# Optimization experiments

Hardware: AMD Instinct MI355X
Metric: run time of the kernel (lower is better)

The kernel has to match this reference:

```python
import jax, jax.numpy as jnp
import numpy as np

N_QUBITS = 10
DIM = 2 ** N_QUBITS          # quantum state dimension
N_LAYERS = 8                 # QAOA circuit depth
B, D_IN, D_HID = 8192, 1024, 2048


def _build_hamiltonians(key):
    """Faithful to _create_cost_hamiltonian / _create_mixer_hamiltonian."""
    k1, k2 = jax.random.split(key)
    # cost: random diagonal * 0.1 plus 100 nearest-neighbour real couplings * 0.05
    diag = (jax.random.normal(k1, (DIM,)) * 0.1).astype(jnp.complex64)
    Hc = jnp.zeros((DIM, DIM), jnp.complex64).at[jnp.arange(DIM), jnp.arange(DIM)].set(diag)
    i = jnp.arange(100)
    j = (i + 1) % DIM
    c = (jax.random.normal(k2, (100,)) * 0.05).astype(jnp.complex64)
    Hc = Hc.at[i, j].set(c).at[j, i].set(jnp.conj(c))
    # mixer: sum of Pauli-X on every qubit -> H[i, i^(1<<q)] += 1
    idx = jnp.arange(DIM)
    Hm = jnp.zeros((DIM, DIM), jnp.complex64)
    for q in range(N_QUBITS):
        Hm = Hm.at[idx, idx ^ (1 << q)].add(1.0)
    return Hc, Hm


def setup_inputs() -> dict:
    key = jax.random.key(0)
    ks = jax.random.split(key, 8)
    Hc, Hm = _build_hamiltonians(ks[0])
    s = lambda k, *sh: jax.random.normal(k, sh, jnp.float32)
    return {
        "x": s(ks[1], B, D_IN),
        "W1": s(ks[2], D_IN, D_HID) * 0.02, "b1": jnp.zeros((D_HID,), jnp.float32),
        "W2": s(ks[3], D_HID, D_HID // 2) * 0.02, "b2": jnp.zeros((D_HID // 2,), jnp.float32),
        "Wq": s(ks[4], N_QUBITS, D_HID // 2) * 0.02, "bq": jnp.zeros((D_HID // 2,), jnp.float32),
        "Wo": s(ks[5], D_HID // 2, D_IN) * 0.02, "bo": jnp.zeros((D_IN,), jnp.float32),
        "circuit_params": s(ks[6], 2 * N_LAYERS),
        "Hc": Hc, "Hm": Hm,
    }


def _qaoa_params(circuit_params, Hc, Hm):
    """QuantumApproximateOptimizer.optimize_parameters: layered unitary evolution
    then a projective measurement mapped to +/-1 parameters."""
    state = jnp.full((DIM,), 1.0 / np.sqrt(DIM), jnp.complex64)
    for l in range(N_LAYERS):  # small fixed layer count -> Python loop OK
        gamma = circuit_params[2 * l].astype(jnp.complex64)
        beta = circuit_params[2 * l + 1].astype(jnp.complex64)
        state = jax.scipy.linalg.expm(-1j * gamma * Hc) @ state
        state = jax.scipy.linalg.expm(-1j * beta * Hm) @ state
    probs = jnp.abs(state) ** 2
    m = jax.random.categorical(jax.random.key(42), jnp.log(probs + 1e-30))
    # format(m, '0{n}b') is MSB-first
    bits = (m >> jnp.arange(N_QUBITS - 1, -1, -1)) & 1
    return bits.astype(jnp.float32) * 2.0 - 1.0  # +/-1 per qubit


def reference(x, W1, b1, W2, b2, Wq, bq, Wo, bo, circuit_params, Hc, Hm):
    # classical encoder: Linear -> ReLU -> Linear
    feat = jax.nn.relu(x @ W1 + b1) @ W2 + b2          # [B, D_HID//2]
    # quantum branch (batch independent)
    qp = _qaoa_params(circuit_params, Hc, Hm)          # [N_QUBITS]
    # surface-code error correction: correction_lookup only maps syndromes
    # '0000'/'1111' to qubit indices 23/24, which fail the `qubit_idx < param_dim`
    # guard for param_dim = N_QUBITS -> provably a no-op; qp unchanged.
    qf = qp @ Wq + bq                                  # [D_HID//2]
    return (feat + qf) @ Wo + bo                       # [B, D_IN]
```

## Files before the change

kernel.cpp:

```cpp
#include <hip/hip_runtime.h>
#include <hip/hip_bf16.h>
#include <stdint.h>

#define DIM 1024
#define NQ 10
#define NLAYERS 8
#define KTAYLOR 16
#define B_ROWS 8192
#define D_IN 1024
#define D_HID 2048
#define D_HALF 1024

typedef __bf16 bf16x8 __attribute__((ext_vector_type(8)));
typedef float f32x4 __attribute__((ext_vector_type(4)));

__device__ __forceinline__ float ldany(const void* p, size_t i, bool f32) {
  if (f32) return ((const float*)p)[i];
  return (float)((const __bf16*)p)[i];
}

__device__ __forceinline__ uint16_t f2bf_bits(float f) {
  __bf16 v = (__bf16)f;
  return *(uint16_t*)&v;
}

__device__ __forceinline__ uint32_t rotl32(uint32_t v, int d) {
  return (v << d) | (v >> (32 - d));
}

__device__ inline void threefry2x32(uint32_t k0, uint32_t k1, uint32_t& x0, uint32_t& x1) {
  uint32_t ks2 = k0 ^ k1 ^ 0x1BD11BDAu;
  x0 += k0; x1 += k1;
#define RND(r) { x0 += x1; x1 = rotl32(x1, r); x1 ^= x0; }
  RND(13) RND(15) RND(26) RND(6)
  x0 += k1; x1 += ks2 + 1u;
  RND(17) RND(29) RND(16) RND(24)
  x0 += ks2; x1 += k0 + 2u;
  RND(13) RND(15) RND(26) RND(6)
  x0 += k0; x1 += k1 + 3u;
  RND(17) RND(29) RND(16) RND(24)
  x0 += k1; x1 += ks2 + 4u;
  RND(13) RND(15) RND(26) RND(6)
  x0 += ks2; x1 += k0 + 5u;
#undef RND
}

__device__ __forceinline__ float gumbel_from_bits(uint32_t b) {
  float f = __uint_as_float((b >> 9) | 0x3f800000u) - 1.0f;
  float u = fmaxf(f, 1.17549435e-38f);
  return -__logf(-__logf(u));
}

struct cplx { double r, i; };
__device__ __forceinline__ cplx load_hc(const void* H, int code, size_t idx) {
  switch (code) {
    case 2: return {(double)((const float*)H)[idx], 0.0};
    case 3: {
      const uint16_t* h = (const uint16_t*)H;
      return {(double)__uint_as_float((uint32_t)h[2 * idx] << 16),
              (double)__uint_as_float((uint32_t)h[2 * idx + 1] << 16)};
    }
    case 4: {
      const double* d = (const double*)H;
      return {d[2 * idx], d[2 * idx + 1]};
    }
    default: {
      float2 v = ((const float2*)H)[idx];
      return {(double)v.x, (double)v.y};
    }
  }
}

__global__ __launch_bounds__(1024) void detect_prep(
    const uint32_t* __restrict__ w1raw, const uint32_t* __restrict__ hc,
    int hcb, const void* __restrict__ b1, const void* __restrict__ bo,
    int* __restrict__ flags, float* __restrict__ b1f,
    float* __restrict__ bias0, float* __restrict__ bias2W) {
  __shared__ int cnt_sh;
  __shared__ int f0_sh;
  const int t = threadIdx.x;
  if (t == 0) cnt_sh = 0;
  __syncthreads();
  if (t < 256) {
    uint16_t h = (uint16_t)(w1raw[t] & 0xFFFFu);
    if (((h >> 7) & 0xFF) >= 0x80) atomicAdd(&cnt_sh, 1);
  }
  __syncthreads();
  if (t == 0) {
    f0_sh = (cnt_sh > 32) ? 1 : 0;
    flags[0] = f0_sh;
    uint32_t w1 = hc[1] & 0x7FFFFFFFu;
    uint32_t w2 = hc[2] & 0x7FFFFFFFu;
    uint32_t w1025 = hc[1025] & 0x7FFFFFFFu;
    int code;
    if (w2 != 0u) code = 1;
    else if (w1 != 0u && (w1 >> 16) == 0u) code = 3;
    else if (w1025 != 0u) code = 2;
    else if (w1 != 0u) code = 4;
    else code = 0;
    flags[1] = code;
  }
  {
    size_t d = (size_t)t * 1025;
    uint32_t a = 0;
    if (8 * d + 4 <= (size_t)hcb) a += hc[2 * d];
    if (4 * d + 4 <= (size_t)hcb) a += hc[d];
    if (16 * d + 4 <= (size_t)hcb) a += hc[4 * d];
    asm volatile("" :: "v"(a));
  }
  __syncthreads();
  const bool f32 = (f0_sh != 0);
  b1f[t] = ldany(b1, t, f32);
  b1f[t + 1024] = ldany(b1, t + 1024, f32);
  bias0[t] = 0.f;
  if (t < 1024) bias0[t + 1024] = 0.f;
  if (t < 1024) bias2W[t] = ldany(bo, t, f32);
}

__global__ void sentinel_kernel(const int* __restrict__ flags,
                                const int* __restrict__ diag,
                                float* __restrict__ out) {
  if (threadIdx.x == 0 && (diag[0] || flags[1] == 0)) {
    out[0] = 1048576.0f + 4194304.0f * (float)diag[0]
           + 65536.0f * (float)flags[1] + 16.0f * (float)diag[1];
  }
}

__device__ void qaoa_body(char* smem,
    const void* __restrict__ Hc_raw, const void* __restrict__ cp,
    const void* __restrict__ b2, const void* __restrict__ bq,
    const void* __restrict__ Wq, const int* __restrict__ flags,
    float* __restrict__ bias2, int* __restrict__ diag) {
  double2* X   = (double2*)smem;
  double* gtab = (double*)(smem + 16384);
  double* cbt  = gtab + 8;
  double* sbt  = cbt + 8;
  float* redv  = (float*)(sbt + 8);
  float* redp  = redv + 4;
  int*   redi  = (int*)(redp + 4);
  int*   bmsh  = redi + 4;

  const int t = threadIdx.x;
  const int lane = t & 63, w = t >> 6;
  const bool f32 = (flags[0] != 0);
  const int code = flags[1];

  double dgr[4], dgi[4];
#pragma unroll
  for (int j = 0; j < 4; ++j) {
    size_t e = (size_t)(w * 256 + j * 64 + lane);
    cplx d = load_hc(Hc_raw, code, e * DIM + e);
    dgr[j] = d.r; dgi[j] = d.i;
  }
  double u0r = 0, u0i = 0, c0r = 0, c0i = 0;
  double u1r = 0, u1i = 0, c1r = 0, c1i = 0;
  if (w == 0) {
    const int e0 = lane, e1 = 64 + lane;
    { cplx u = load_hc(Hc_raw, code, (size_t)e0 * DIM + e0 + 1); u0r = u.r; u0i = u.i; }
    if (e0 >= 1)  { cplx c = load_hc(Hc_raw, code, (size_t)e0 * DIM + e0 - 1); c0r = c.r; c0i = c.i; }
    if (e1 <= 100){ cplx u = load_hc(Hc_raw, code, (size_t)e1 * DIM + e1 + 1); u1r = u.r; u1i = u.i; }
    if (e1 <= 101){ cplx c = load_hc(Hc_raw, code, (size_t)e1 * DIM + e1 - 1); c1r = c.r; c1i = c.i; }
  }
  if (t < NLAYERS) {
    gtab[t] = (double)ldany(cp, 2 * t, f32);
    double b = (double)ldany(cp, 2 * t + 1, f32), s, c;
    sincos(b, &s, &c);
    cbt[t] = c; sbt[t] = s;
  }
  double ar[4], ai[4];
#pragma unroll
  for (int j = 0; j < 4; ++j) { ar[j] = 0.03125; ai[j] = 0.0; }
  __syncthreads();

  for (int l = 0; l < NLAYERS; ++l) {
    const double gamma = gtab[l];
    const double cb = cbt[l], sb = sbt[l];
    const double cb2 = cb * cb, cbsb = cb * sb, sb2 = sb * sb;

    if (w == 0) {
      double p0r = ar[0], p0i = ai[0], p1r = ar[1], p1i = ai[1];
      double y0r = p0r, y0i = p0i, y1r = p1r, y1i = p1i;
#pragma unroll
      for (int k = 1; k <= KTAYLOR; ++k) {
        double a0r = __shfl_down(p0r, 1), a0i = __shfl_down(p0i, 1);
        double a1r = __shfl_down(p1r, 1), a1i = __shfl_down(p1i, 1);
        double m0r = __shfl_up(p0r, 1),   m0i = __shfl_up(p0i, 1);
        double m1r = __shfl_up(p1r, 1),   m1i = __shfl_up(p1i, 1);
        double b0r = __shfl(p1r, 0),  b0i = __shfl(p1i, 0);
        double b1r = __shfl(p0r, 63), b1i = __shfl(p0i, 63);
        if (lane == 63) { a0r = b0r; a0i = b0i; }
        if (lane == 0)  { m1r = b1r; m1i = b1i; }
        double h0r = dgr[0]*p0r - dgi[0]*p0i + u0r*a0r - u0i*a0i + c0r*m0r - c0i*m0i;
        double h0i = dgr[0]*p0i + dgi[0]*p0r + u0r*a0i + u0i*a0r + c0r*m0i + c0i*m0r;
        double h1r = dgr[1]*p1r - dgi[1]*p1i + u1r*a1r - u1i*a1i + c1r*m1r - c1i*m1i;
        double h1i = dgr[1]*p1i + dgi[1]*p1r + u1r*a1i + u1i*a1r + c1r*m1i + c1i*m1r;
        const double s = gamma * (1.0 / (double)k);
        p0r = s * h0i; p0i = -s * h0r;
        p1r = s * h1i; p1i = -s * h1r;
        y0r += p0r; y0i += p0i; y1r += p1r; y1i += p1i;
      }
      ar[0] = y0r; ai[0] = y0i; ar[1] = y1r; ai[1] = y1i;
#pragma unroll
      for (int j = 2; j < 4; ++j) {
        float angf = (float)(gamma * dgr[j]);
        double sn = (double)__sinf(angf), cs = (double)__cosf(angf);
        double sc_ = (dgi[j] == 0.0) ? 1.0 : exp(gamma * dgi[j]);
        double nr = sc_ * (ar[j] * cs + ai[j] * sn);
        double ni = sc_ * (ai[j] * cs - ar[j] * sn);
        ar[j] = nr; ai[j] = ni;
      }
    } else {
#pragma unroll
      for (int j = 0; j < 4; ++j) {
        float angf = (float)(gamma * dgr[j]);
        double sn = (double)__sinf(angf), cs = (double)__cosf(angf);
        double sc_ = (dgi[j] == 0.0) ? 1.0 : exp(gamma * dgi[j]);
        double nr = sc_ * (ar[j] * cs + ai[j] * sn);
        double ni = sc_ * (ai[j] * cs - ar[j] * sn);
        ar[j] = nr; ai[j] = ni;
      }
    }

#pragma unroll
    for (int s2 = 0; s2 < 3; ++s2) {
      const int mA = 1 << (2 * s2), mB = 2 << (2 * s2), mC = 3 << (2 * s2);
#pragma unroll
      for (int j = 0; j < 4; ++j) {
        double pr1 = __shfl_xor(ar[j], mA), pi1 = __shfl_xor(ai[j], mA);
        double pr2 = __shfl_xor(ar[j], mB), pi2 = __shfl_xor(ai[j], mB);
        double pr3 = __shfl_xor(ar[j], mC), pi3 = __shfl_xor(ai[j], mC);
        double nr = cb2 * ar[j] + cbsb * (pi1 + pi2) - sb2 * pr3;
        double ni = cb2 * ai[j] - cbsb * (pr1 + pr2) - sb2 * pi3;
        ar[j] = nr; ai[j] = ni;
      }
    }
    {
      double nr[4], ni[4];
#pragma unroll
      for (int j = 0; j < 4; ++j) {
        nr[j] = cb2 * ar[j] + cbsb * (ai[j ^ 1] + ai[j ^ 2]) - sb2 * ar[j ^ 3];
        ni[j] = cb2 * ai[j] - cbsb * (ar[j ^ 1] + ar[j ^ 2]) - sb2 * ai[j ^ 3];
      }
#pragma unroll
      for (int j = 0; j < 4; ++j) { ar[j] = nr[j]; ai[j] = ni[j]; }
    }
    {
#pragma unroll
      for (int j = 0; j < 4; ++j)
        X[w * 256 + j * 64 + lane] = make_double2(ar[j], ai[j]);
      __syncthreads();
#pragma unroll
      for (int j = 0; j < 4; ++j) {
        int e = w * 256 + j * 64 + lane;
        double2 vb = X[e ^ 256], vc = X[e ^ 512], vd = X[e ^ 768];
        double nr = cb2 * ar[j] + cbsb * (vb.y + vc.y) - sb2 * vd.x;
        double ni = cb2 * ai[j] - cbsb * (vb.x + vc.x) - sb2 * vd.y;
        ar[j] = nr; ai[j] = ni;
      }
      __syncthreads();
    }
  }

  float best = -1e30f; int bidx = 0; float pv = 0.f;
#pragma unroll
  for (int j = 0; j < 4; ++j) {
    int e = w * 256 + j * 64 + lane;
    double prob = ar[j] * ar[j] + ai[j] * ai[j];
    pv += (float)prob;
    float logit = __logf((float)prob + 1e-30f);
    uint32_t x0 = 0u, x1 = (uint32_t)e;
    threefry2x32(0u, 42u, x0, x1);
    float sc = logit + gumbel_from_bits(x0 ^ x1);
    if (sc > best) { best = sc; bidx = e; }
  }
#pragma unroll
  for (int off = 32; off >= 1; off >>= 1) {
    float ov = __shfl_down(best, off);
    int oi = __shfl_down(bidx, off);
    pv += __shfl_down(pv, off);
    if (ov > best) { best = ov; bidx = oi; }
  }
  if (lane == 0) { redv[w] = best; redi[w] = bidx; redp[w] = pv; }
  __syncthreads();
  if (t == 0) {
    float bb = redv[0]; int bm = redi[0]; float tot = redp[0];
    for (int k = 1; k < 4; ++k) {
      tot += redp[k];
      if (redv[k] > bb) { bb = redv[k]; bm = redi[k]; }
    }
    bmsh[0] = bm;
    diag[0] = (!(tot > 0.99f && tot < 1.01f)) ? 1 : 0;
    diag[1] = bm;
  }
  __syncthreads();
  const int m = bmsh[0];

#pragma unroll
  for (int k4 = 0; k4 < 4; ++k4) {
    int c = t + 256 * k4;
    float acc = ldany(b2, c, f32) + ldany(bq, c, f32);
#pragma unroll
    for (int k = 0; k < NQ; ++k) {
      float qp = ((m >> (9 - k)) & 1) ? 1.f : -1.f;
      acc += qp * ldany(Wq, (size_t)k * D_HALF + c, f32);
    }
    bias2[c] = acc;
  }
}

__device__ void transpose_body(char* smem, const void* __restrict__ in,
                               uint16_t* __restrict__ out, int R, int C,
                               bool f32, int bxi, int byi) {
  uint16_t (*tile)[33] = (uint16_t(*)[33])smem;
  int bc = bxi * 32, br = byi * 32;
  int x = threadIdx.x & 31, y = threadIdx.x >> 5;
#pragma unroll
  for (int i = 0; i < 4; ++i) {
    int r = y * 4 + i;
    size_t idx = (size_t)(br + r) * C + bc + x;
    tile[r][x] = f32 ? f2bf_bits(((const float*)in)[idx])
                     : ((const uint16_t*)in)[idx];
  }
  __syncthreads();
#pragma unroll
  for (int i = 0; i < 4; ++i) {
    int c = y * 4 + i;
    out[(size_t)(bc + c) * R + br + x] = tile[x][c];
  }
}

__device__ void convert_body(const void* __restrict__ src,
                             __bf16* __restrict__ dst, int n, bool f32, int b) {
  int i = (b * 256 + (int)threadIdx.x) * 8;
  if (i >= n) return;
  if (f32) {
    const float* s = (const float*)src + i;
#pragma unroll
    for (int j = 0; j < 8; ++j) dst[i + j] = (__bf16)s[j];
  } else {
    *(uint4*)(dst + i) = *(const uint4*)((const uint16_t*)src + i);
  }
}

__global__ __launch_bounds__(256) void mega_prep(
    const void* __restrict__ Hc, const void* __restrict__ cp,
    const void* __restrict__ b2, const void* __restrict__ bq,
    const void* __restrict__ Wq, const int* __restrict__ flags,
    float* __restrict__ bias2, int* __restrict__ diag,
    const void* __restrict__ W1, uint16_t* __restrict__ W1T,
    const void* __restrict__ Wo, uint16_t* __restrict__ WoT,
    const void* __restrict__ W2, __bf16* __restrict__ W2bf,
    const void* __restrict__ x, __bf16* __restrict__ xc, int nx) {
  __shared__ __align__(16) char smem[16640];
  int b = blockIdx.x;
  if (b == 0) {
    qaoa_body(smem, Hc, cp, b2, bq, Wq, flags, bias2, diag);
    return;
  }
  const bool f32 = (flags[0] != 0);
  b -= 1;
  if (b < 2048) {
    transpose_body(smem, W1, W1T, 1024, 2048, f32, b & 63, b >> 6);
    return;
  }
  b -= 2048;
  if (b < 1024) {
    transpose_body(smem, Wo, WoT, 1024, 1024, f32, b & 31, b >> 5);
    return;
  }
  b -= 1024;
  if (b < 1024) {
    convert_body(W2, W2bf, 2048 * 1024, f32, b);
    return;
  }
  b -= 1024;
  if (b < nx)
    convert_body(x, xc, nx * 2048, f32, b);
}

__global__ __launch_bounds__(256) void convert_bf16(
    const void* __restrict__ src, size_t soff, __bf16* __restrict__ dst,
    int n, const int* __restrict__ flags) {
  int i = (blockIdx.x * 256 + threadIdx.x) * 8;
  if (i >= n) return;
  if (flags[0]) {
    const float* s = (const float*)src + soff + i;
#pragma unroll
    for (int j = 0; j < 8; ++j) dst[i + j] = (__bf16)s[j];
  } else {
    *(uint4*)(dst + i) = *(const uint4*)((const uint16_t*)src + soff + i);
  }
}

__global__ __launch_bounds__(256) void fold_bias(
    const float* __restrict__ bias2, const void* __restrict__ Wo,
    const int* __restrict__ flags, float* __restrict__ bias2W) {
  const bool f32 = (flags[0] != 0);
  const int kb = blockIdx.x * 32;
  const int c = threadIdx.x;
  float s0 = 0.f, s1 = 0.f, s2 = 0.f, s3 = 0.f;
#pragma unroll 4
  for (int k = kb; k < kb + 32; ++k) {
    float bk = bias2[k];
    s0 += bk * ldany(Wo, (size_t)k * 1024 + c,       f32);
    s1 += bk * ldany(Wo, (size_t)k * 1024 + c + 256, f32);
    s2 += bk * ldany(Wo, (size_t)k * 1024 + c + 512, f32);
    s3 += bk * ldany(Wo, (size_t)k * 1024 + c + 768, f32);
  }
  atomicAdd(&bias2W[c],       s0);
  atomicAdd(&bias2W[c + 256], s1);
  atomicAdd(&bias2W[c + 512], s2);
  atomicAdd(&bias2W[c + 768], s3);
}

__device__ __forceinline__ void stage_tile(
    const __bf16* __restrict__ G, int row0, int K, int k0,
    __bf16* lds, int wave, int lane) {
#pragma unroll
  for (int r = 0; r < 2; ++r) {
    int row  = r * 64 + wave * 16 + (lane >> 2);
    int slot = (lane & 3) ^ ((row >> 1) & 3);
    const __bf16* gp = G + (size_t)(row0 + row) * K + k0 + slot * 8;
    __builtin_amdgcn_global_load_lds(
        (const __attribute__((address_space(1))) void*)gp,
        (__attribute__((address_space(3))) void*)(lds + r * 2048 + wave * 512),
        16, 0, 0);
  }
}

template <bool RELU, bool OUTF32>
__global__ __launch_bounds__(256) void gemm_bt(
    const __bf16* __restrict__ A, const __bf16* __restrict__ Bt,
    const float* __restrict__ bias, void* __restrict__ Cout,
    int N, int K) {
  __shared__ __bf16 Als[3][128 * 32];
  __shared__ __bf16 Bls[3][128 * 32];

  const int tid = threadIdx.x;
  const int wave = tid >> 6, lane = tid & 63;

  const int gx = gridDim.x;
  const int nwg = gx * gridDim.y;
  int flat = blockIdx.y * gx + blockIdx.x;
  const int chunk = nwg >> 3;
  flat = (flat & 7) * chunk + (flat >> 3);
  const int m0 = (flat / gx) * 128, n0 = (flat % gx) * 128;

  const int wm = (wave >> 1) * 64, wn = (wave & 1) * 64;
  const int lm = lane & 15, quad = lane >> 4;

  f32x4 acc[4][4] = {};

  const int nt = K >> 5;
  stage_tile(A,  m0, K, 0,  Als[0], wave, lane);
  stage_tile(Bt, n0, K, 0,  Bls[0], wave, lane);
  stage_tile(A,  m0, K, 32, Als[1], wave, lane);
  stage_tile(Bt, n0, K, 32, Bls[1], wave, lane);

  int cur = 0;
  for (int t = 0; t < nt; ++t) {
    if (t == nt - 1)
      asm volatile("s_waitcnt vmcnt(0)\n\ts_barrier" ::: "memory");
    else
      asm volatile("s_waitcnt vmcnt(4)\n\ts_barrier" ::: "memory");

    if (t + 2 < nt) {
      int nb = cur + 2; if (nb >= 3) nb -= 3;
      stage_tile(A,  m0, K, (t + 2) << 5, Als[nb], wave, lane);
      stage_tile(Bt, n0, K, (t + 2) << 5, Bls[nb], wave, lane);
    }

    bf16x8 af[4], bfr[4];
#pragma unroll
    for (int i = 0; i < 4; ++i) {
      int row = wm + i * 16 + lm;
      af[i] = *(const bf16x8*)(Als[cur] + row * 32 +
                               (quad ^ ((row >> 1) & 3)) * 8);
    }
#pragma unroll
    for (int i = 0; i < 4; ++i) {
      int row = wn + i * 16 + lm;
      bfr[i] = *(const bf16x8*)(Bls[cur] + row * 32 +
                                (quad ^ ((row >> 1) & 3)) * 8);
    }
#pragma unroll
    for (int mi = 0; mi < 4; ++mi)
#pragma unroll
      for (int ni = 0; ni < 4; ++ni)
        acc[mi][ni] = __builtin_amdgcn_mfma_f32_16x16x32_bf16(
            af[mi], bfr[ni], acc[mi][ni], 0, 0, 0);

    if (++cur >= 3) cur = 0;
  }

#pragma unroll
  for (int mi = 0; mi < 4; ++mi) {
#pragma unroll
    for (int ni = 0; ni < 4; ++ni) {
      int col = n0 + wn + ni * 16 + lm;
      float bv = bias[col];
#pragma unroll
      for (int r = 0; r < 4; ++r) {
        int row = m0 + wm + mi * 16 + quad * 4 + r;
        float v = acc[mi][ni][r] + bv;
        if (RELU) v = fmaxf(v, 0.f);
        size_t oi = (size_t)row * N + col;
        if (OUTF32) ((float*)Cout)[oi] = v;
        else        ((__bf16*)Cout)[oi] = (__bf16)v;
      }
    }
  }
}

extern "C" void kernel_launch(void* const* d_in, const int* in_sizes, int n_in,
                              void* d_out, int out_size, void* d_ws, size_t ws_size,
                              hipStream_t stream) {
  const void* x  = d_in[0];
  const void* W1 = d_in[1];
  const void* b1 = d_in[2];
  const void* W2 = d_in[3];
  const void* b2 = d_in[4];
  const void* Wq = d_in[5];
  const void* bq = d_in[6];
  const void* Wo = d_in[7];
  const void* bo = d_in[8];
  const void* cp = d_in[9];
  const void* Hc = d_in[10];
  float* out = (float*)d_out;

  char* ws = (char*)d_ws;
  float* b1f    = (float*)ws;
  float* bias2W = (float*)(ws + 8192);
  float* bias0  = (float*)(ws + 12288);
  float* bias2  = (float*)(ws + 20480);
  int*   flags  = (int*)(ws + 24576);
  int*   diag   = (int*)(ws + 24576 + 64);
  __bf16* W1T   = (__bf16*)(ws + 32768);
  __bf16* W2bf  = W1T + (size_t)2048 * 1024;
  __bf16* WoT   = W2bf + (size_t)2048 * 1024;
  __bf16* W2WoT = WoT + (size_t)1024 * 1024;
  const size_t head = 32768 + (size_t)14 * 1024 * 1024;
  int R = B_ROWS;
  while (R > 128 && head + (size_t)R * 6144 > ws_size) R >>= 1;
  __bf16* xc   = (__bf16*)(ws + head);
  __bf16* Hbuf = xc + (size_t)R * 1024;

  detect_prep<<<1, 1024, 0, stream>>>((const uint32_t*)W1, (const uint32_t*)Hc,
                                      in_sizes[10], b1, bo, flags, b1f, bias0,
                                      bias2W);

  const int nx = R / 2;
  mega_prep<<<1 + 2048 + 1024 + 1024 + nx, 256, 0, stream>>>(
      Hc, cp, b2, bq, Wq, flags, bias2, diag,
      W1, (uint16_t*)W1T, Wo, (uint16_t*)WoT, W2, W2bf, x, xc, nx);

  fold_bias<<<32, 256, 0, stream>>>(bias2, Wo, flags, bias2W);

  gemm_bt<false, false><<<dim3(2048 / 128, 1024 / 128), 256, 0, stream>>>(
      WoT, W2bf, bias0, W2WoT, 2048, 1024);

  for (int off = 0; off < B_ROWS; off += R) {
    if (off > 0) {
      int nconv = R * 1024;
      convert_bf16<<<(nconv / 8 + 255) / 256, 256, 0, stream>>>(
          x, (size_t)off * D_IN, xc, nconv, flags);
    }
    gemm_bt<true, false><<<dim3(D_HID / 128, R / 128), 256, 0, stream>>>(
        xc, W1T, b1f, Hbuf, D_HID, D_IN);
    gemm_bt<false, true><<<dim3(D_IN / 128, R / 128), 256, 0, stream>>>(
        Hbuf, W2WoT, bias2W, out + (size_t)off * D_IN, D_IN, D_HID);
  }

  sentinel_kernel<<<1, 64, 0, stream>>>(flags, diag, out);
}
```

Measured before the change: 282.1 us.

## Use fp32 QAOA simulation and fuse first GEMM, weight-fold GEMM and bias fold

The QAOA state-vector simulation moves from double to single precision, cutting slow FP64 arithmetic, shuffles and shared-memory traffic in the single-block serial prep stage. Separately, the first-chunk x@W1 GEMM, the Wo·W2 weight-fold GEMM and the bias-fold kernel now run in one launch, dispatched by block index. This removes two launches and lets the small independent jobs fill idle CUs alongside the big GEMM. The cost is lower precision in the state evolution, which could change the sampled bitstring, and a kernel whose blocks do uneven work.

Result: slower. 309.4 us (+9.7%).

```diff
diff --git a/kernel.cpp b/kernel.cpp
--- a/kernel.cpp
+++ b/kernel.cpp
@@ -131,70 +131,70 @@
     const void* __restrict__ b2, const void* __restrict__ bq,
     const void* __restrict__ Wq, const int* __restrict__ flags,
     float* __restrict__ bias2, int* __restrict__ diag) {
-  double2* X   = (double2*)smem;
-  double* gtab = (double*)(smem + 16384);
-  double* cbt  = gtab + 8;
-  double* sbt  = cbt + 8;
-  float* redv  = (float*)(sbt + 8);
-  float* redp  = redv + 4;
-  int*   redi  = (int*)(redp + 4);
-  int*   bmsh  = redi + 4;
+  float2* X   = (float2*)smem;
+  float* gtab = (float*)(smem + 8192);
+  float* cbt  = gtab + 8;
+  float* sbt  = cbt + 8;
+  float* redv = sbt + 8;
+  float* redp = redv + 4;
+  int*   redi = (int*)(redp + 4);
+  int*   bmsh = redi + 4;
 
   const int t = threadIdx.x;
   const int lane = t & 63, w = t >> 6;
   const bool f32 = (flags[0] != 0);
   const int code = flags[1];
 
-  double dgr[4], dgi[4];
+  float dgr[4], dgi[4];
 #pragma unroll
   for (int j = 0; j < 4; ++j) {
     size_t e = (size_t)(w * 256 + j * 64 + lane);
     cplx d = load_hc(Hc_raw, code, e * DIM + e);
-    dgr[j] = d.r; dgi[j] = d.i;
-  }
-  double u0r = 0, u0i = 0, c0r = 0, c0i = 0;
-  double u1r = 0, u1i = 0, c1r = 0, c1i = 0;
+    dgr[j] = (float)d.r; dgi[j] = (float)d.i;
+  }
+  float u0r = 0, u0i = 0, c0r = 0, c0i = 0;
+  float u1r = 0, u1i = 0, c1r = 0, c1i = 0;
   if (w == 0) {
     const int e0 = lane, e1 = 64 + lane;
-    { cplx u = load_hc(Hc_raw, code, (size_t)e0 * DIM + e0 + 1); u0r = u.r; u0i = u.i; }
-    if (e0 >= 1)  { cplx c = load_hc(Hc_raw, code, (size_t)e0 * DIM + e0 - 1); c0r = c.r; c0i = c.i; }
-    if (e1 <= 100){ cplx u = load_hc(Hc_raw, code, (size_t)e1 * DIM + e1 + 1); u1r = u.r; u1i = u.i; }
-    if (e1 <= 101){ cplx c = load_hc(Hc_raw, code, (size_t)e1 * DIM + e1 - 1); c1r = c.r; c1i = c.i; }
+    { cplx u = load_hc(Hc_raw, code, (size_t)e0 * DIM + e0 + 1); u0r = (float)u.r; u0i = (float)u.i; }
+    if (e0 >= 1)  { cplx c = load_hc(Hc_raw, code, (size_t)e0 * DIM + e0 - 1); c0r = (float)c.r; c0i = (float)c.i; }
+    if (e1 <= 100){ cplx u = load_hc(Hc_raw, code, (size_t)e1 * DIM + e1 + 1); u1r = (float)u.r; u1i = (float)u.i; }
+    if (e1 <= 101){ cplx c = load_hc(Hc_raw, code, (size_t)e1 * DIM + e1 - 1); c1r = (float)c.r; c1i = (float)c.i; }
   }
   if (t < NLAYERS) {
-    gtab[t] = (double)ldany(cp, 2 * t, f32);
+    gtab[t] = ldany(cp, 2 * t, f32);
     double b = (double)ldany(cp, 2 * t + 1, f32), s, c;
     sincos(b, &s, &c);
-    cbt[t] = c; sbt[t] = s;
-  }
-  double ar[4], ai[4];
-#pragma unroll
-  for (int j = 0; j < 4; ++j) { ar[j] = 0.03125; ai[j] = 0.0; }
+    cbt[t] = (float)c; sbt[t] = (float)s;
+  }
+  float ar[4], ai[4];
+#pragma unroll
+  for (int j = 0; j < 4; ++j) { ar[j] = 0.03125f; ai[j] = 0.0f; }
   __syncthreads();
 
   for (int l = 0; l < NLAYERS; ++l) {
-    const double gamma = gtab[l];
-    const double cb = cbt[l], sb = sbt[l];
-    const double cb2 = cb * cb, cbsb = cb * sb, sb2 = sb * sb;
+    const float gamma = gtab[l];
+    const float cb = cbt[l], sb = sbt[l];
+    const float cb2 = cb * cb, cbsb = cb * sb, sb2 = sb * sb;
 
     if (w == 0) {
-      double p0r = ar[0], p0i = ai[0], p1r = ar[1], p1i = ai[1];
-      double y0r = p0r, y0i = p0i, y1r = p1r, y1i = p1i;
+      float p0r = ar[0], p0i = ai[0], p1r = ar[1], p1i = ai[1];
+      float y0r = p0r, y0i = p0i, y1r = p1r, y1i = p1i;
 #pragma unroll
       for (int k = 1; k <= KTAYLOR; ++k) {
-        double a0r = __shfl_down(p0r, 1), a0i = __shfl_down(p0i, 1);
-        double a1r = __shfl_down(p1r, 1), a1i = __shfl_down(p1i, 1);
-        double m0r = __shfl_up(p0r, 1),   m0i = __shfl_up(p0i, 1);
-        double m1r = __shfl_up(p1r, 1),   m1i = __shfl_up(p1i, 1);
-        double b0r = __shfl(p1r, 0),  b0i = __shfl(p1i, 0);
-        double b1r = __shfl(p0r, 63), b1i = __shfl(p0i, 63);
+        float a0r = __shfl_down(p0r, 1), a0i = __shfl_down(p0i, 1);
+        float a1r = __shfl_down(p1r, 1), a1i = __shfl_down(p1i, 1);
+        float m0r = __shfl_up(p0r, 1),   m0i = __shfl_up(p0i, 1);
+        float m1r = __shfl_up(p1r, 1),   m1i = __shfl_up(p1i, 1);
+        float b0r = __shfl(p1r, 0),  b0i = __shfl(p1i, 0);
+        float b1r = __shfl(p0r, 63), b1i = __shfl(p0i, 63);
         if (lane == 63) { a0r = b0r; a0i = b0i; }
         if (lane == 0)  { m1r = b1r; m1i = b1i; }
-        double h0r = dgr[0]*p0r - dgi[0]*p0i + u0r*a0r - u0i*a0i + c0r*m0r - c0i*m0i;
-        double h0i = dgr[0]*p0i + dgi[0]*p0r + u0r*a0i + u0i*a0r + c0r*m0i + c0i*m0r;
-        double h1r = dgr[1]*p1r - dgi[1]*p1i + u1r*a1r - u1i*a1i + c1r*m1r - c1i*m1i;
-        double h1i = dgr[1]*p1i + dgi[1]*p1r + u1r*a1i + u1i*a1r + c1r*m1i + c1i*m1r;
-        const double s = gamma * (1.0 / (double)k);
+        float h0r = dgr[0]*p0r - dgi[0]*p0i + u0r*a0r - u0i*a0i + c0r*m0r - c0i*m0i;
+        float h0i = dgr[0]*p0i + dgi[0]*p0r + u0r*a0i + u0i*a0r + c0r*m0i + c0i*m0r;
+        float h1r = dgr[1]*p1r - dgi[1]*p1i + u1r*a1r - u1i*a1i + c1r*m1r - c1i*m1i;
+        float h1i = dgr[1]*p1i + dgi[1]*p1r + u1r*a1i + u1i*a1r + c1r*m1i + c1i*m1r;
+        const float s = gamma * (1.0f / (float)k);
         p0r = s * h0i; p0i = -s * h0r;
         p1r = s * h1i; p1i = -s * h1r;
         y0r += p0r; y0i += p0i; y1r += p1r; y1i += p1i;
@@ -202,21 +202,21 @@
       ar[0] = y0r; ai[0] = y0i; ar[1] = y1r; ai[1] = y1i;
 #pragma unroll
       for (int j = 2; j < 4; ++j) {
-        float angf = (float)(gamma * dgr[j]);
-        double sn = (double)__sinf(angf), cs = (double)__cosf(angf);
-        double sc_ = (dgi[j] == 0.0) ? 1.0 : exp(gamma * dgi[j]);
-        double nr = sc_ * (ar[j] * cs + ai[j] * sn);
-        double ni = sc_ * (ai[j] * cs - ar[j] * sn);
+        float ang = gamma * dgr[j];
+        float sn = __sinf(ang), cs = __cosf(ang);
+        float sc_ = (dgi[j] == 0.0f) ? 1.0f : __expf(gamma * dgi[j]);
+        float nr = sc_ * (ar[j] * cs + ai[j] * sn);
+        float ni = sc_ * (ai[j] * cs - ar[j] * sn);
         ar[j] = nr; ai[j] = ni;
       }
     } else {
 #pragma unroll
       for (int j = 0; j < 4; ++j) {
-        float angf = (float)(gamma * dgr[j]);
-        double sn = (double)__sinf(angf), cs = (double)__cosf(angf);
-        double sc_ = (dgi[j] == 0.0) ? 1.0 : exp(gamma * dgi[j]);
-        double nr = sc_ * (ar[j] * cs + ai[j] * sn);
-        double ni = sc_ * (ai[j] * cs - ar[j] * sn);
+        float ang = gamma * dgr[j];
+        float sn = __sinf(ang), cs = __cosf(ang);
+        float sc_ = (dgi[j] == 0.0f) ? 1.0f : __expf(gamma * dgi[j]);
+        float nr = sc_ * (ar[j] * cs + ai[j] * sn);
+        float ni = sc_ * (ai[j] * cs - ar[j] * sn);
         ar[j] = nr; ai[j] = ni;
       }
     }
@@ -226,16 +226,16 @@
       const int mA = 1 << (2 * s2), mB = 2 << (2 * s2), mC = 3 << (2 * s2);
 #pragma unroll
       for (int j = 0; j < 4; ++j) {
-        double pr1 = __shfl_xor(ar[j], mA), pi1 = __shfl_xor(ai[j], mA);
-        double pr2 = __shfl_xor(ar[j], mB), pi2 = __shfl_xor(ai[j], mB);
-        double pr3 = __shfl_xor(ar[j], mC), pi3 = __shfl_xor(ai[j], mC);
-        double nr = cb2 * ar[j] + cbsb * (pi1 + pi2) - sb2 * pr3;
-        double ni = cb2 * ai[j] - cbsb * (pr1 + pr2) - sb2 * pi3;
+        float pr1 = __shfl_xor(ar[j], mA), pi1 = __shfl_xor(ai[j], mA);
+        float pr2 = __shfl_xor(ar[j], mB), pi2 = __shfl_xor(ai[j], mB);
+        float pr3 = __shfl_xor(ar[j], mC), pi3 = __shfl_xor(ai[j], mC);
+        float nr = cb2 * ar[j] + cbsb * (pi1 + pi2) - sb2 * pr3;
+        float ni = cb2 * ai[j] - cbsb * (pr1 + pr2) - sb2 * pi3;
         ar[j] = nr; ai[j] = ni;
       }
     }
     {
-      double nr[4], ni[4];
+      float nr[4], ni[4];
 #pragma unroll
       for (int j = 0; j < 4; ++j) {
         nr[j] = cb2 * ar[j] + cbsb * (ai[j ^ 1] + ai[j ^ 2]) - sb2 * ar[j ^ 3];
@@ -247,14 +247,14 @@
     {
 #pragma unroll
       for (int j = 0; j < 4; ++j)
-        X[w * 256 + j * 64 + lane] = make_double2(ar[j], ai[j]);
+        X[w * 256 + j * 64 + lane] = make_float2(ar[j], ai[j]);
       __syncthreads();
 #pragma unroll
       for (int j = 0; j < 4; ++j) {
         int e = w * 256 + j * 64 + lane;
-        double2 vb = X[e ^ 256], vc = X[e ^ 512], vd = X[e ^ 768];
-        double nr = cb2 * ar[j] + cbsb * (vb.y + vc.y) - sb2 * vd.x;
-        double ni = cb2 * ai[j] - cbsb * (vb.x + vc.x) - sb2 * vd.y;
+        float2 vb = X[e ^ 256], vc = X[e ^ 512], vd = X[e ^ 768];
+        float nr = cb2 * ar[j] + cbsb * (vb.y + vc.y) - sb2 * vd.x;
+        float ni = cb2 * ai[j] - cbsb * (vb.x + vc.x) - sb2 * vd.y;
         ar[j] = nr; ai[j] = ni;
       }
       __syncthreads();
@@ -265,9 +265,9 @@
 #pragma unroll
   for (int j = 0; j < 4; ++j) {
     int e = w * 256 + j * 64 + lane;
-    double prob = ar[j] * ar[j] + ai[j] * ai[j];
-    pv += (float)prob;
-    float logit = __logf((float)prob + 1e-30f);
+    float prob = ar[j] * ar[j] + ai[j] * ai[j];
+    pv += prob;
+    float logit = __logf(prob + 1e-30f);
     uint32_t x0 = 0u, x1 = (uint32_t)e;
     threefry2x32(0u, 42u, x0, x1);
     float sc = logit + gumbel_from_bits(x0 ^ x1);
@@ -392,11 +392,12 @@
   }
 }
 
-__global__ __launch_bounds__(256) void fold_bias(
-    const float* __restrict__ bias2, const void* __restrict__ Wo,
-    const int* __restrict__ flags, float* __restrict__ bias2W) {
+__device__ void fold_body(const float* __restrict__ bias2,
+                          const void* __restrict__ Wo,
+                          const int* __restrict__ flags,
+                          float* __restrict__ bias2W, int blk) {
   const bool f32 = (flags[0] != 0);
-  const int kb = blockIdx.x * 32;
+  const int kb = blk * 32;
   const int c = threadIdx.x;
   float s0 = 0.f, s1 = 0.f, s2 = 0.f, s3 = 0.f;
 #pragma unroll 4
@@ -428,21 +429,14 @@
   }
 }
 
-template <bool RELU, bool OUTF32>
-__global__ __launch_bounds__(256) void gemm_bt(
+__device__ void gemm_body(__bf16* Als, __bf16* Bls,
     const __bf16* __restrict__ A, const __bf16* __restrict__ Bt,
     const float* __restrict__ bias, void* __restrict__ Cout,
-    int N, int K) {
-  __shared__ __bf16 Als[3][128 * 32];
-  __shared__ __bf16 Bls[3][128 * 32];
-
+    int N, int K, int flat, int gx, int ntiles, bool relu, bool outf32) {
   const int tid = threadIdx.x;
   const int wave = tid >> 6, lane = tid & 63;
 
-  const int gx = gridDim.x;
-  const int nwg = gx * gridDim.y;
-  int flat = blockIdx.y * gx + blockIdx.x;
-  const int chunk = nwg >> 3;
+  const int chunk = ntiles >> 3;
   flat = (flat & 7) * chunk + (flat >> 3);
   const int m0 = (flat / gx) * 128, n0 = (flat % gx) * 128;
 
@@ -452,10 +446,10 @@
   f32x4 acc[4][4] = {};
 
   const int nt = K >> 5;
-  stage_tile(A,  m0, K, 0,  Als[0], wave, lane);
-  stage_tile(Bt, n0, K, 0,  Bls[0], wave, lane);
-  stage_tile(A,  m0, K, 32, Als[1], wave, lane);
-  stage_tile(Bt, n0, K, 32, Bls[1], wave, lane);
+  stage_tile(A,  m0, K, 0,  Als, wave, lane);
+  stage_tile(Bt, n0, K, 0,  Bls, wave, lane);
+  stage_tile(A,  m0, K, 32, Als + 4096, wave, lane);
+  stage_tile(Bt, n0, K, 32, Bls + 4096, wave, lane);
 
   int cur = 0;
   for (int t = 0; t < nt; ++t) {
@@ -466,21 +460,21 @@
 
     if (t + 2 < nt) {
       int nb = cur + 2; if (nb >= 3) nb -= 3;
-      stage_tile(A,  m0, K, (t + 2) << 5, Als[nb], wave, lane);
-      stage_tile(Bt, n0, K, (t + 2) << 5, Bls[nb], wave, lane);
+      stage_tile(A,  m0, K, (t + 2) << 5, Als + nb * 4096, wave, lane);
+      stage_tile(Bt, n0, K, (t + 2) << 5, Bls + nb * 4096, wave, lane);
     }
 
     bf16x8 af[4], bfr[4];
 #pragma unroll
     for (int i = 0; i < 4; ++i) {
       int row = wm + i * 16 + lm;
-      af[i] = *(const bf16x8*)(Als[cur] + row * 32 +
+      af[i] = *(const bf16x8*)(Als + cur * 4096 + row * 32 +
                                (quad ^ ((row >> 1) & 3)) * 8);
     }
 #pragma unroll
     for (int i = 0; i < 4; ++i) {
       int row = wn + i * 16 + lm;
-      bfr[i] = *(const bf16x8*)(Bls[cur] + row * 32 +
+      bfr[i] = *(const bf16x8*)(Bls + cur * 4096 + row * 32 +
                                 (quad ^ ((row >> 1) & 3)) * 8);
     }
 #pragma unroll
@@ -503,13 +497,51 @@
       for (int r = 0; r < 4; ++r) {
         int row = m0 + wm + mi * 16 + quad * 4 + r;
         float v = acc[mi][ni][r] + bv;
-        if (RELU) v = fmaxf(v, 0.f);
+        if (relu) v = fmaxf(v, 0.f);
         size_t oi = (size_t)row * N + col;
-        if (OUTF32) ((float*)Cout)[oi] = v;
+        if (outf32) ((float*)Cout)[oi] = v;
         else        ((__bf16*)Cout)[oi] = (__bf16)v;
       }
     }
   }
+}
+
+template <bool RELU, bool OUTF32>
+__global__ __launch_bounds__(256) void gemm_bt(
+    const __bf16* __restrict__ A, const __bf16* __restrict__ Bt,
+    const float* __restrict__ bias, void* __restrict__ Cout,
+    int N, int K) {
+  __shared__ __bf16 Als[3 * 128 * 32];
+  __shared__ __bf16 Bls[3 * 128 * 32];
+  int flat = blockIdx.y * gridDim.x + blockIdx.x;
+  gemm_body(Als, Bls, A, Bt, bias, Cout, N, K, flat, gridDim.x,
+            gridDim.x * gridDim.y, RELU, OUTF32);
+}
+
+__global__ __launch_bounds__(256) void gemm_plus(
+    const __bf16* __restrict__ xc, const __bf16* __restrict__ W1T,
+    const float* __restrict__ b1f, __bf16* __restrict__ Hbuf,
+    const __bf16* __restrict__ WoT, const __bf16* __restrict__ W2bf,
+    const float* __restrict__ bias0, __bf16* __restrict__ W2WoT,
+    const float* __restrict__ bias2, const void* __restrict__ Wo,
+    const int* __restrict__ flags, float* __restrict__ bias2W,
+    int g1_tiles) {
+  __shared__ __bf16 Als[3 * 128 * 32];
+  __shared__ __bf16 Bls[3 * 128 * 32];
+  int b = blockIdx.x;
+  if (b < g1_tiles) {
+    gemm_body(Als, Bls, xc, W1T, b1f, Hbuf, 2048, 1024, b, 16, g1_tiles,
+              true, false);
+    return;
+  }
+  b -= g1_tiles;
+  if (b < 128) {
+    gemm_body(Als, Bls, WoT, W2bf, bias0, W2WoT, 2048, 1024, b, 16, 128,
+              false, false);
+    return;
+  }
+  b -= 128;
+  fold_body(bias2, Wo, flags, bias2W, b);
 }
 
 extern "C" void kernel_launch(void* const* d_in, const int* in_sizes, int n_in,
@@ -554,19 +586,19 @@
       Hc, cp, b2, bq, Wq, flags, bias2, diag,
       W1, (uint16_t*)W1T, Wo, (uint16_t*)WoT, W2, W2bf, x, xc, nx);
 
-  fold_bias<<<32, 256, 0, stream>>>(bias2, Wo, flags, bias2W);
-
-  gemm_bt<false, false><<<dim3(2048 / 128, 1024 / 128), 256, 0, stream>>>(
-      WoT, W2bf, bias0, W2WoT, 2048, 1024);
+  const int g1_tiles = (R / 128) * 16;
+  gemm_plus<<<g1_tiles + 128 + 32, 256, 0, stream>>>(
+      xc, W1T, b1f, Hbuf, WoT, W2bf, bias0, W2WoT,
+      bias2, Wo, flags, bias2W, g1_tiles);
 
   for (int off = 0; off < B_ROWS; off += R) {
     if (off > 0) {
       int nconv = R * 1024;
       convert_bf16<<<(nconv / 8 + 255) / 256, 256, 0, stream>>>(
           x, (size_t)off * D_IN, xc, nconv, flags);
-    }
-    gemm_bt<true, false><<<dim3(D_HID / 128, R / 128), 256, 0, stream>>>(
-        xc, W1T, b1f, Hbuf, D_HID, D_IN);
+      gemm_bt<true, false><<<dim3(D_HID / 128, R / 128), 256, 0, stream>>>(
+          xc, W1T, b1f, Hbuf, D_HID, D_IN);
+    }
     gemm_bt<false, true><<<dim3(D_IN / 128, R / 128), 256, 0, stream>>>(
         Hbuf, W2WoT, bias2W, out + (size_t)off * D_IN, D_IN, D_HID);
   }
```
